# Kernel optimization log

Hardware: AMD Instinct MI355X
Metric: run time of the kernel (lower is better)

Reference implementation:

```python
import jax, jax.numpy as jnp
import numpy as np

B, T, X, H, Z, G, Y = 4096, 32, 256, 256, 256, 128, 2


def _xavier(key, fan_in, fan_out):
    lim = float(np.sqrt(6.0 / (fan_in + fan_out)))
    return jax.random.uniform(key, (fan_in, fan_out), jnp.float32, -lim, lim)


def setup_inputs() -> dict:
    key = jax.random.key(0)
    ks = jax.random.split(key, 18)
    return {
        "x": jax.random.normal(ks[0], (B, T, X), jnp.float32),
        "y_ph": jax.random.uniform(ks[1], (B, T, Y), jnp.float32),
        "T_ph": jax.random.randint(ks[2], (B,), 1, T + 1),  # 1..T valid days
        "h0": jnp.tanh(jax.random.normal(ks[3], (B, H), jnp.float32)),   # tanh(randn) init state
        "z0": jnp.tanh(jax.random.normal(ks[4], (B, Z), jnp.float32)),
        "eps": jax.random.normal(ks[5], (T, B, Z), jnp.float32),          # reparam noise per step
        # gate / candidate nets: fan_in = x + h + z
        "Wr": _xavier(ks[6], X + H + Z, H), "br": jnp.zeros((H,), jnp.float32),
        "Wu": _xavier(ks[7], X + H + Z, H), "bu": jnp.zeros((H,), jnp.float32),
        "Wh": _xavier(ks[8], X + H + Z, H), "bh": jnp.zeros((H,), jnp.float32),
        # prior latent net: fan_in = x + h
        "Wzp": _xavier(ks[9], X + H, Z), "bzp": jnp.zeros((Z,), jnp.float32),
        "Wpm": _xavier(ks[10], Z, Z), "bpm": jnp.zeros((Z,), jnp.float32),
        "Wps": _xavier(ks[11], Z, Z), "bps": jnp.zeros((Z,), jnp.float32),
        # posterior latent net: fan_in = x + h + y
        "Wzq": _xavier(ks[12], X + H + Y, Z), "bzq": jnp.zeros((Z,), jnp.float32),
        "Wqm": _xavier(ks[13], Z, Z), "bqm": jnp.zeros((Z,), jnp.float32),
        "Wqs": _xavier(ks[14], Z, Z), "bqs": jnp.zeros((Z,), jnp.float32),
        # output nets
        "Wg": _xavier(ks[15], X + H + Z, G), "bg": jnp.zeros((G,), jnp.float32),
        "Wy": _xavier(ks[16], G, Y), "by": jnp.zeros((Y,), jnp.float32),
    }


def reference(x, y_ph, T_ph, h0, z0, eps,
              Wr, br, Wu, bu, Wh, bh,
              Wzp, bzp, Wpm, bpm, Wps, bps,
              Wzq, bzq, Wqm, bqm, Wqs, bqs,
              Wg, bg, Wy, by):
    x_t = jnp.transpose(x, (1, 0, 2))     # [T, B, X]
    y_t = jnp.transpose(y_ph, (1, 0, 2))  # [T, B, Y]

    def step(carry, inp):
        h_prev, z_prev = carry
        xt, yt, et = inp
        ga = jnp.concatenate([xt, h_prev, z_prev], axis=-1)
        r = jax.nn.sigmoid(ga @ Wr + br)
        u = jax.nn.sigmoid(ga @ Wu + bu)
        ha = jnp.concatenate([xt, r * h_prev, z_prev], axis=-1)
        h_tilde = jnp.tanh(ha @ Wh + bh)
        h = (1.0 - u) * h_prev + u * h_tilde
        # prior p(z_t | x_t, h_t): z_prior = mean (is_prior=True)
        hzp = jnp.tanh(jnp.concatenate([xt, h], axis=-1) @ Wzp + bzp)
        mu_p = hzp @ Wpm + bpm
        sd_p = jnp.sqrt(jnp.exp(hzp @ Wps + bps))
        z_prior = mu_p
        # posterior q(z_t | x_t, h_t, y_t): reparameterized sample
        hzq = jnp.tanh(jnp.concatenate([xt, h, yt], axis=-1) @ Wzq + bzq)
        mu_q = hzq @ Wqm + bqm
        sd_q = jnp.sqrt(jnp.exp(hzq @ Wqs + bqs))
        z_post = mu_q + sd_q * et
        # KL(q || p) for diagonal Normals
        kl = jnp.log(sd_p / sd_q) + (sd_q ** 2 + (mu_q - mu_p) ** 2) / (2.0 * sd_p ** 2) - 0.5
        return (h, z_post), (h, z_post, z_prior, kl)

    (_, _), (h_s, z_post, z_prior, kl) = jax.lax.scan(step, (h0, z0), (x_t, y_t, eps))
    h_s = jnp.transpose(h_s, (1, 0, 2))      # [B, T, H]
    z_post = jnp.transpose(z_post, (1, 0, 2))
    kl = jnp.transpose(kl, (1, 0, 2)).sum(axis=-1)  # [B, T]

    g = jnp.tanh(jnp.concatenate([x, h_s, z_post], axis=-1) @ Wg + bg)  # [B, T, G]
    y = jax.nn.softmax(g @ Wy + by, axis=-1)                             # [B, T, Y]
    g_T = g[jnp.arange(x.shape[0]), T_ph - 1]                            # [B, G] (training, daily_att)
    return (y, kl, g_T)
```

## Files before the change

kernel.cpp:

```cpp
#include <hip/hip_runtime.h>

typedef unsigned short u16;
typedef unsigned int u32;
typedef __attribute__((ext_vector_type(8))) short short8;
typedef __attribute__((ext_vector_type(4))) float float4v;
typedef __attribute__((ext_vector_type(2))) float float2v;

#define B_SZ 4096
#define T_SZ 32
#define XD 256
#define HD 256
#define ZD 256
#define GD 128
#define YD 2

#define BM 64
#define NW 16

#define W1_OFF 0
#define W2_OFF 393216
#define W3_OFF 589824
#define W4_OFF 868352
#define WG_OFF 1130496
#define WTOT   1228800

#define YTOT  (B_SZ*T_SZ*YD)
#define KLTOT (B_SZ*T_SZ)

#define UST 264

__device__ __forceinline__ u16 f2bf(float f) {
    u32 u = __float_as_uint(f);
    u32 r = (u + 0x7fffu + ((u >> 16) & 1u)) >> 16;
    return (u16)r;
}
__device__ __forceinline__ float bf2f(u16 h) {
    return __uint_as_float(((u32)h) << 16);
}
__device__ __forceinline__ float tanh_f(float x) {
    float e = __expf(2.f * x);
    return 1.f - 2.f / (e + 1.f);
}
__device__ __forceinline__ float sigm_f(float x) {
    return 1.f / (1.f + __expf(-x));
}

__device__ __forceinline__ int aga_off(int r, int k) {
    return (((r >> 4) * 24 + (k >> 5)) << 9) + ((((k >> 3) & 3) * 16 + (r & 15)) << 3) + (k & 7);
}
__device__ __forceinline__ int a3h_off(int r, int k, int pq) {
    return (((pq * 2 + (r >> 4)) * 8 + (k >> 5)) << 9) + ((((k >> 3) & 3) * 16 + (r & 15)) << 3) + (k & 7);
}

#define MFMA(a, b, c) __builtin_amdgcn_mfma_f32_16x16x32_bf16(a, b, c, 0, 0, 0)

__global__ void prep_weights(const float* __restrict__ Wr, const float* __restrict__ Wu,
                             const float* __restrict__ Wh, const float* __restrict__ Wzp,
                             const float* __restrict__ Wzq, const float* __restrict__ Wpm,
                             const float* __restrict__ Wps, const float* __restrict__ Wqm,
                             const float* __restrict__ Wqs, const float* __restrict__ Wg,
                             u16* __restrict__ wts)
{
    int o = blockIdx.x * 256 + threadIdx.x;
    if (o >= WTOT) return;
    int mat, w, KT;
    if (o < W2_OFF)      { mat = 0; w = o;          KT = 24; }
    else if (o < W3_OFF) { mat = 1; w = o - W2_OFF; KT = 24; }
    else if (o < W4_OFF) { mat = 2; w = o - W3_OFF; KT = 17; }
    else if (o < WG_OFF) { mat = 3; w = o - W4_OFF; KT = 8;  }
    else                 { mat = 4; w = o - WG_OFF; KT = 24; }
    int nt  = w / (KT * 512);
    int rem = w - nt * (KT * 512);
    int kt  = rem >> 9;
    int q   = rem & 511;
    int lane = q >> 3, j = q & 7;
    int n = (nt << 4) | (lane & 15);
    int k = (kt << 5) + ((lane >> 4) << 3) + j;
    float v = 0.f;
    switch (mat) {
        case 0: v = (n < 256) ? Wr[k * 256 + n] : Wu[k * 256 + (n - 256)]; break;
        case 1: v = Wh[k * 256 + n]; break;
        case 2: v = (n < 256) ? (k < 512 ? Wzp[k * 256 + n] : 0.f)
                              : (k < 514 ? Wzq[k * 256 + (n - 256)] : 0.f); break;
        case 3: { int sel = n >> 8; int nn = n & 255;
                  const float* s = (sel == 0) ? Wpm : (sel == 1) ? Wps : (sel == 2) ? Wqm : Wqs;
                  v = s[k * 256 + nn]; } break;
        default: v = Wg[k * 128 + n]; break;
    }
    wts[o] = f2bf(v);
}

__global__ __launch_bounds__(1024, 4) void vrnn_all(
    const float* __restrict__ x,   const float* __restrict__ y_ph,
    const int*   __restrict__ Tph, const float* __restrict__ h0,
    const float* __restrict__ z0,  const float* __restrict__ eps,
    const float* __restrict__ br,  const float* __restrict__ bu,
    const float* __restrict__ bh,  const float* __restrict__ bzp,
    const float* __restrict__ bpm, const float* __restrict__ bps,
    const float* __restrict__ bzq, const float* __restrict__ bqm,
    const float* __restrict__ bqs, const float* __restrict__ bg,
    const float* __restrict__ by,  const float* __restrict__ Wy,
    const u16*   __restrict__ wts, float* __restrict__ out)
{
    __shared__ __align__(16) u16   a_ga[96 * 512];
    __shared__ __align__(16) u16   a3u[16896];
    __shared__ float part[8 * BM * 2];
    __shared__ float kl_acc[BM];
    __shared__ int   tph_s[BM];

    const int tid  = threadIdx.x;
    const int wv   = tid >> 6;
    const int lane = tid & 63;
    const int quad = lane >> 4;
    const int l15  = lane & 15;
    const int b0   = blockIdx.x * BM;

    const int c10 = wv * 32 + l15;
    const float bs1_0 = (c10 < 256) ? br[c10] : bu[c10 - 256];
    const float bs1_1 = (c10 + 16 < 256) ? br[c10 + 16] : bu[c10 + 16 - 256];
    const int c2  = wv * 16 + l15;
    const float bh_r  = bh[c2];
    const float bzp_r = bzp[c2];
    const float bzq_r = bzq[c2];
    const float b4pm = bpm[c2], b4ps = bps[c2], b4qm = bqm[c2], b4qs = bqs[c2];
    const int c5  = (wv >> 1) * 16 + l15;
    const int mt5 = wv & 1;
    const float bg_r = bg[c5];
    const float wy0 = Wy[c5 * 2], wy1 = Wy[c5 * 2 + 1];
    const float by0 = by[0], by1 = by[1];

    if (tid < BM) tph_s[tid] = Tph[b0 + tid];

    float h32r[16];
#pragma unroll
    for (int m = 0; m < 4; ++m)
#pragma unroll
        for (int i = 0; i < 4; ++i) {
            int row = m * 16 + quad * 4 + i;
            h32r[m * 4 + i] = __builtin_nontemporal_load(&h0[(size_t)(b0 + row) * HD + c2]);
        }

    const int sr  = tid >> 4;
    const int scc = (tid & 15) * 16;

    float4v xn[4];
    {
        const float* xp = &x[((size_t)(b0 + sr) * T_SZ + 0) * XD + scc];
#pragma unroll
        for (int q = 0; q < 4; ++q) xn[q] = __builtin_nontemporal_load((const float4v*)(xp + q * 4));

        const float* hp = &h0[(size_t)(b0 + sr) * HD + scc];
        const float* zp = &z0[(size_t)(b0 + sr) * ZD + scc];
        float4v hv[4], zv[4];
#pragma unroll
        for (int q = 0; q < 4; ++q) {
            hv[q] = __builtin_nontemporal_load((const float4v*)(hp + q * 4));
            zv[q] = __builtin_nontemporal_load((const float4v*)(zp + q * 4));
        }
        short8 hs0, hs1, zs0, zs1;
#pragma unroll
        for (int j = 0; j < 4; ++j) {
            hs0[j] = (short)f2bf(hv[0][j]); hs0[4 + j] = (short)f2bf(hv[1][j]);
            hs1[j] = (short)f2bf(hv[2][j]); hs1[4 + j] = (short)f2bf(hv[3][j]);
            zs0[j] = (short)f2bf(zv[0][j]); zs0[4 + j] = (short)f2bf(zv[1][j]);
            zs1[j] = (short)f2bf(zv[2][j]); zs1[4 + j] = (short)f2bf(zv[3][j]);
        }
        *(short8*)&a_ga[aga_off(sr, 256 + scc)]     = hs0;
        *(short8*)&a_ga[aga_off(sr, 256 + scc + 8)] = hs1;
        *(short8*)&a_ga[aga_off(sr, 512 + scc)]     = zs0;
        *(short8*)&a_ga[aga_off(sr, 512 + scc + 8)] = zs1;
    }
    __syncthreads();

    const float4v zero4 = {0.f, 0.f, 0.f, 0.f};
    float yA0 = 0.f, yA1 = 0.f, yB0 = 0.f, yB1 = 0.f, klA = 0.f, klB = 0.f;

    for (int t = 0; t < T_SZ; ++t) {
        {
            short8 s0, s1;
#pragma unroll
            for (int j = 0; j < 4; ++j) {
                s0[j] = (short)f2bf(xn[0][j]); s0[4 + j] = (short)f2bf(xn[1][j]);
                s1[j] = (short)f2bf(xn[2][j]); s1[4 + j] = (short)f2bf(xn[3][j]);
            }
            *(short8*)&a_ga[aga_off(sr, scc)]     = s0;
            *(short8*)&a_ga[aga_off(sr, scc + 8)] = s1;
        }
        __syncthreads();

        {
            const u16* pB0 = wts + W1_OFF + (((2 * wv    ) * 24) << 9) + lane * 8;
            const u16* pB1 = wts + W1_OFF + (((2 * wv + 1) * 24) << 9) + lane * 8;
            short8 r0[2], r1[2];
            r0[0] = *(const short8*)pB0;         r1[0] = *(const short8*)pB1;
            r0[1] = *(const short8*)(pB0 + 512); r1[1] = *(const short8*)(pB1 + 512);
            float4v a0[4], a1[4];
#pragma unroll
            for (int m = 0; m < 4; ++m) { a0[m] = zero4; a1[m] = zero4; }
#pragma unroll
            for (int kt = 0; kt < 24; ++kt) {
                short8 bc0 = r0[kt & 1], bc1 = r1[kt & 1];
                if (kt + 2 < 24) {
                    r0[kt & 1] = *(const short8*)(pB0 + ((kt + 2) << 9));
                    r1[kt & 1] = *(const short8*)(pB1 + ((kt + 2) << 9));
                }
#pragma unroll
                for (int m = 0; m < 4; ++m) {
                    short8 aF = *(const short8*)&a_ga[((m * 24 + kt) << 9) + lane * 8];
                    a0[m] = MFMA(aF, bc0, a0[m]);
                    a1[m] = MFMA(aF, bc1, a1[m]);
                }
            }
            __syncthreads();
#pragma unroll
            for (int m = 0; m < 4; ++m)
#pragma unroll
                for (int i = 0; i < 4; ++i) {
                    int row = m * 16 + quad * 4 + i;
                    {
                        float v = a0[m][i];
                        if (c10 < 256) {
                            int o = aga_off(row, 256 + c10);
                            float rr = sigm_f(v + bs1_0);
                            a_ga[o] = f2bf(rr * bf2f(a_ga[o]));
                        } else {
                            a3u[row * UST + (c10 - 256)] = f2bf(sigm_f(v + bs1_0));
                        }
                    }
                    {
                        int c = c10 + 16;
                        float v = a1[m][i];
                        if (c < 256) {
                            int o = aga_off(row, 256 + c);
                            float rr = sigm_f(v + bs1_1);
                            a_ga[o] = f2bf(rr * bf2f(a_ga[o]));
                        } else {
                            a3u[row * UST + (c - 256)] = f2bf(sigm_f(v + bs1_1));
                        }
                    }
                }
            __syncthreads();
        }

        {
            const u16* pB = wts + W2_OFF + ((wv * 24) << 9) + lane * 8;
            short8 rr2[2];
            rr2[0] = *(const short8*)pB; rr2[1] = *(const short8*)(pB + 512);
            float4v a[4];
#pragma unroll
            for (int m = 0; m < 4; ++m) a[m] = zero4;
#pragma unroll
            for (int kt = 0; kt < 24; ++kt) {
                short8 bc = rr2[kt & 1];
                if (kt + 2 < 24) rr2[kt & 1] = *(const short8*)(pB + ((kt + 2) << 9));
#pragma unroll
                for (int m = 0; m < 4; ++m) {
                    short8 aF = *(const short8*)&a_ga[((m * 24 + kt) << 9) + lane * 8];
                    a[m] = MFMA(aF, bc, a[m]);
                }
            }
            __syncthreads();
#pragma unroll
            for (int m = 0; m < 4; ++m)
#pragma unroll
                for (int i = 0; i < 4; ++i) {
                    int row = m * 16 + quad * 4 + i;
                    float ht = tanh_f(a[m][i] + bh_r);
                    float uu = bf2f(a3u[row * UST + c2]);
                    float h  = (1.f - uu) * h32r[m * 4 + i] + uu * ht;
                    h32r[m * 4 + i] = h;
                    a_ga[aga_off(row, 256 + c2)] = f2bf(h);
                }
            if (tid < 256) {
                int r = tid >> 2, grp = tid & 3;
                short8 v = {0, 0, 0, 0, 0, 0, 0, 0};
                if (grp == 0) {
                    const float* yp = &y_ph[((size_t)(b0 + r) * T_SZ + t) * YD];
                    v[0] = (short)f2bf(__builtin_nontemporal_load(yp));
                    v[1] = (short)f2bf(__builtin_nontemporal_load(yp + 1));
                }
                *(short8*)&a_ga[aga_off(r, 512 + grp * 8)] = v;
            }
            __syncthreads();
        }

#pragma unroll
        for (int half = 0; half < 2; ++half) {
            {
                const u16* pBp = wts + W3_OFF + ((wv * 17) << 9) + lane * 8;
                const u16* pBq = wts + W3_OFF + (((16 + wv) * 17) << 9) + lane * 8;
                short8 rp[2], rq[2];
                rp[0] = *(const short8*)pBp; rp[1] = *(const short8*)(pBp + 512);
                rq[0] = *(const short8*)pBq; rq[1] = *(const short8*)(pBq + 512);
                float4v aP[2], aQ[2];
                aP[0] = zero4; aP[1] = zero4; aQ[0] = zero4; aQ[1] = zero4;
#pragma unroll
                for (int kt = 0; kt < 17; ++kt) {
                    short8 bq = rq[kt & 1];
                    short8 bp = rp[kt & 1];
                    if (kt + 2 < 17) rq[kt & 1] = *(const short8*)(pBq + ((kt + 2) << 9));
                    if (kt + 2 < 16) rp[kt & 1] = *(const short8*)(pBp + ((kt + 2) << 9));
#pragma unroll
                    for (int m2 = 0; m2 < 2; ++m2) {
                        short8 aF = *(const short8*)&a_ga[(((half * 2 + m2) * 24 + kt) << 9) + lane * 8];
                        aQ[m2] = MFMA(aF, bq, aQ[m2]);
                        if (kt < 16) aP[m2] = MFMA(aF, bp, aP[m2]);
                    }
                }
                if (half == 0 && tid < BM) kl_acc[tid] = 0.f;
#pragma unroll
                for (int m2 = 0; m2 < 2; ++m2)
#pragma unroll
                    for (int i = 0; i < 4; ++i) {
                        int r5 = m2 * 16 + quad * 4 + i;
                        a3u[a3h_off(r5, c2, 0)] = f2bf(tanh_f(aP[m2][i] + bzp_r));
                        a3u[a3h_off(r5, c2, 1)] = f2bf(tanh_f(aQ[m2][i] + bzq_r));
                    }
                __syncthreads();
            }
            {
                const u16* pB0 = wts + W4_OFF + (((      wv) * 8) << 9) + lane * 8;
                const u16* pB1 = wts + W4_OFF + (((16 + wv) * 8) << 9) + lane * 8;
                const u16* pB2 = wts + W4_OFF + (((32 + wv) * 8) << 9) + lane * 8;
                const u16* pB3 = wts + W4_OFF + (((48 + wv) * 8) << 9) + lane * 8;
                float er8[8];
#pragma unroll
                for (int m2 = 0; m2 < 2; ++m2)
#pragma unroll
                    for (int i = 0; i < 4; ++i) {
                        int row = half * 32 + m2 * 16 + quad * 4 + i;
                        er8[m2 * 4 + i] = __builtin_nontemporal_load(
                            &eps[((size_t)t * B_SZ + (b0 + row)) * ZD + c2]);
                    }
                short8 r0[2], r1[2], r2[2], r3[2];
                r0[0] = *(const short8*)pB0;         r1[0] = *(const short8*)pB1;
                r2[0] = *(const short8*)pB2;         r3[0] = *(const short8*)pB3;
                r0[1] = *(const short8*)(pB0 + 512); r1[1] = *(const short8*)(pB1 + 512);
                r2[1] = *(const short8*)(pB2 + 512); r3[1] = *(const short8*)(pB3 + 512);
                float4v amp[2], asp[2], amq[2], asq[2];
                amp[0] = zero4; amp[1] = zero4; asp[0] = zero4; asp[1] = zero4;
                amq[0] = zero4; amq[1] = zero4; asq[0] = zero4; asq[1] = zero4;
#pragma unroll
                for (int kt = 0; kt < 8; ++kt) {
                    short8 b0c = r0[kt & 1], b1c = r1[kt & 1];
                    short8 b2c = r2[kt & 1], b3c = r3[kt & 1];
                    if (kt + 2 < 8) {
                        r0[kt & 1] = *(const short8*)(pB0 + ((kt + 2) << 9));
                        r1[kt & 1] = *(const short8*)(pB1 + ((kt + 2) << 9));
                        r2[kt & 1] = *(const short8*)(pB2 + ((kt + 2) << 9));
                        r3[kt & 1] = *(const short8*)(pB3 + ((kt + 2) << 9));
                    }
#pragma unroll
                    for (int m2 = 0; m2 < 2; ++m2) {
                        short8 aP = *(const short8*)&a3u[(((m2    ) * 8 + kt) << 9) + lane * 8];
                        short8 aQ = *(const short8*)&a3u[(((2 + m2) * 8 + kt) << 9) + lane * 8];
                        amp[m2] = MFMA(aP, b0c, amp[m2]); asp[m2] = MFMA(aP, b1c, asp[m2]);
                        amq[m2] = MFMA(aQ, b2c, amq[m2]); asq[m2] = MFMA(aQ, b3c, asq[m2]);
                    }
                }
#pragma unroll
                for (int m2 = 0; m2 < 2; ++m2)
#pragma unroll
                    for (int i = 0; i < 4; ++i) {
                        int row = half * 32 + m2 * 16 + quad * 4 + i;
                        float mp = amp[m2][i] + b4pm;
                        float sp = asp[m2][i] + b4ps;
                        float mq = amq[m2][i] + b4qm;
                        float sq = asq[m2][i] + b4qs;
                        float zpost = mq + __expf(0.5f * sq) * er8[m2 * 4 + i];
                        float dmu = mq - mp;
                        float kl = 0.5f * (sp - sq)
                                 + (__expf(sq) + dmu * dmu) * 0.5f * __expf(-sp) - 0.5f;
                        a_ga[aga_off(row, 512 + c2)] = f2bf(zpost);
                        kl += __shfl_xor(kl, 1); kl += __shfl_xor(kl, 2);
                        kl += __shfl_xor(kl, 4); kl += __shfl_xor(kl, 8);
                        if (l15 == 0) atomicAdd(&kl_acc[row], kl);
                    }
                __syncthreads();
            }
        }
        if ((tid & 15) == (t >> 1)) {
            float k = kl_acc[tid >> 4];
            if ((t & 1) == 0) klA = k; else klB = k;
        }

        {
            if (t + 1 < T_SZ) {
                const float* xp = &x[((size_t)(b0 + sr) * T_SZ + (t + 1)) * XD + scc];
#pragma unroll
                for (int q = 0; q < 4; ++q)
                    xn[q] = __builtin_nontemporal_load((const float4v*)(xp + q * 4));
            }
            const u16* pB = wts + WG_OFF + (((wv >> 1) * 24) << 9) + lane * 8;
            short8 rg[2];
            rg[0] = *(const short8*)pB; rg[1] = *(const short8*)(pB + 512);
            float4v a5[2];
            a5[0] = zero4; a5[1] = zero4;
#pragma unroll
            for (int kt = 0; kt < 24; ++kt) {
                short8 bc = rg[kt & 1];
                if (kt + 2 < 24) rg[kt & 1] = *(const short8*)(pB + ((kt + 2) << 9));
                short8 aFa = *(const short8*)&a_ga[(((mt5    ) * 24 + kt) << 9) + lane * 8];
                short8 aFb = *(const short8*)&a_ga[(((mt5 + 2) * 24 + kt) << 9) + lane * 8];
                a5[0] = MFMA(aFa, bc, a5[0]);
                a5[1] = MFMA(aFb, bc, a5[1]);
            }
#pragma unroll
            for (int half = 0; half < 2; ++half) {
                int m = mt5 + 2 * half;
#pragma unroll
                for (int i = 0; i < 4; ++i) {
                    int row = m * 16 + quad * 4 + i;
                    float g = tanh_f(a5[half][i] + bg_r);
                    if (tph_s[row] - 1 == t)
                        __builtin_nontemporal_store(g,
                            &out[YTOT + KLTOT + (size_t)(b0 + row) * GD + c5]);
                    float p0 = g * wy0, p1 = g * wy1;
                    p0 += __shfl_xor(p0, 1); p0 += __shfl_xor(p0, 2);
                    p0 += __shfl_xor(p0, 4); p0 += __shfl_xor(p0, 8);
                    p1 += __shfl_xor(p1, 1); p1 += __shfl_xor(p1, 2);
                    p1 += __shfl_xor(p1, 4); p1 += __shfl_xor(p1, 8);
                    if (l15 == 0) {
                        part[((wv >> 1) * BM + row) * 2]     = p0;
                        part[((wv >> 1) * BM + row) * 2 + 1] = p1;
                    }
                }
            }
            __syncthreads();
            if ((tid & 15) == (t >> 1)) {
                int r = tid >> 4;
                float s0 = by0, s1 = by1;
#pragma unroll
                for (int j = 0; j < 8; ++j) {
                    s0 += part[(j * BM + r) * 2];
                    s1 += part[(j * BM + r) * 2 + 1];
                }
                float mx = fmaxf(s0, s1);
                float e0 = __expf(s0 - mx), e1 = __expf(s1 - mx);
                float inv = 1.f / (e0 + e1);
                if ((t & 1) == 0) { yA0 = e0 * inv; yA1 = e1 * inv; }
                else              { yB0 = e0 * inv; yB1 = e1 * inv; }
            }
        }
    }

    {
        int r = tid >> 4, tt = tid & 15;
        float4v yv = {yA0, yA1, yB0, yB1};
        __builtin_nontemporal_store(yv,
            (float4v*)&out[((size_t)(b0 + r) * T_SZ + tt * 2) * YD]);
        float2v kv = {klA, klB};
        __builtin_nontemporal_store(kv,
            (float2v*)&out[YTOT + (size_t)(b0 + r) * T_SZ + tt * 2]);
    }
}

extern "C" void kernel_launch(void* const* d_in, const int* in_sizes, int n_in,
                              void* d_out, int out_size, void* d_ws, size_t ws_size,
                              hipStream_t stream)
{
    const float* x   = (const float*)d_in[0];
    const float* yph = (const float*)d_in[1];
    const int*   Tph = (const int*)  d_in[2];
    const float* h0  = (const float*)d_in[3];
    const float* z0  = (const float*)d_in[4];
    const float* eps = (const float*)d_in[5];
    const float* Wr  = (const float*)d_in[6];
    const float* br  = (const float*)d_in[7];
    const float* Wu  = (const float*)d_in[8];
    const float* bu  = (const float*)d_in[9];
    const float* Wh  = (const float*)d_in[10];
    const float* bh  = (const float*)d_in[11];
    const float* Wzp = (const float*)d_in[12];
    const float* bzp = (const float*)d_in[13];
    const float* Wpm = (const float*)d_in[14];
    const float* bpm = (const float*)d_in[15];
    const float* Wps = (const float*)d_in[16];
    const float* bps = (const float*)d_in[17];
    const float* Wzq = (const float*)d_in[18];
    const float* bzq = (const float*)d_in[19];
    const float* Wqm = (const float*)d_in[20];
    const float* bqm = (const float*)d_in[21];
    const float* Wqs = (const float*)d_in[22];
    const float* bqs = (const float*)d_in[23];
    const float* Wg  = (const float*)d_in[24];
    const float* bg  = (const float*)d_in[25];
    const float* Wy  = (const float*)d_in[26];
    const float* by  = (const float*)d_in[27];
    u16*   wts = (u16*)d_ws;
    float* out = (float*)d_out;

    hipLaunchKernelGGL(prep_weights, dim3((WTOT + 255) / 256), dim3(256), 0, stream,
                       Wr, Wu, Wh, Wzp, Wzq, Wpm, Wps, Wqm, Wqs, Wg, wts);
    hipLaunchKernelGGL(vrnn_all, dim3(B_SZ / BM), dim3(1024), 0, stream,
                       x, yph, Tph, h0, z0, eps, br, bu, bh, bzp, bpm, bps,
                       bzq, bqm, bqs, bg, by, Wy, wts, out);
}
```

Baseline: 4.662 ms.

## Halve batch tile to 32 rows with 8 waves, widening per-wave column tiles

Each block now handles 32 batch rows with 512 threads (8 waves) instead of 64 rows with 1024 threads. Each wave covers twice as many output columns, and the weight-prefetch depth grows from 2 to 4 k-steps. The posterior/prior stage now runs in one pass instead of two halves. This doubles the grid and is meant to improve occupancy and latency hiding of the sequential per-step GEMMs. The cost is that weight traffic per batch row doubles, since each block re-streams the full weight set for half as many rows, and register pressure rises.

```diff
diff --git a/kernel.cpp b/kernel.cpp
--- a/kernel.cpp
+++ b/kernel.cpp
@@ -14,8 +14,8 @@
 #define GD 128
 #define YD 2
 
-#define BM 64
-#define NW 16
+#define BM 32
+#define NW 8
 
 #define W1_OFF 0
 #define W2_OFF 393216
@@ -48,7 +48,7 @@
 __device__ __forceinline__ int aga_off(int r, int k) {
     return (((r >> 4) * 24 + (k >> 5)) << 9) + ((((k >> 3) & 3) * 16 + (r & 15)) << 3) + (k & 7);
 }
-__device__ __forceinline__ int a3h_off(int r, int k, int pq) {
+__device__ __forceinline__ int a3s_off(int r, int k, int pq) {
     return (((pq * 2 + (r >> 4)) * 8 + (k >> 5)) << 9) + ((((k >> 3) & 3) * 16 + (r & 15)) << 3) + (k & 7);
 }
 
@@ -90,7 +90,7 @@
     wts[o] = f2bf(v);
 }
 
-__global__ __launch_bounds__(1024, 4) void vrnn_all(
+__global__ __launch_bounds__(512, 2) void vrnn_all(
     const float* __restrict__ x,   const float* __restrict__ y_ph,
     const int*   __restrict__ Tph, const float* __restrict__ h0,
     const float* __restrict__ z0,  const float* __restrict__ eps,
@@ -102,9 +102,9 @@
     const float* __restrict__ by,  const float* __restrict__ Wy,
     const u16*   __restrict__ wts, float* __restrict__ out)
 {
-    __shared__ __align__(16) u16   a_ga[96 * 512];
-    __shared__ __align__(16) u16   a3u[16896];
-    __shared__ float part[8 * BM * 2];
+    __shared__ __align__(16) u16   a_ga[48 * 512];
+    __shared__ __align__(16) u16   a3s[32 * 512];
+    __shared__ float part[NW * BM * 2];
     __shared__ float kl_acc[BM];
     __shared__ int   tph_s[BM];
 
@@ -115,30 +115,40 @@
     const int l15  = lane & 15;
     const int b0   = blockIdx.x * BM;
 
-    const int c10 = wv * 32 + l15;
-    const float bs1_0 = (c10 < 256) ? br[c10] : bu[c10 - 256];
-    const float bs1_1 = (c10 + 16 < 256) ? br[c10 + 16] : bu[c10 + 16 - 256];
-    const int c2  = wv * 16 + l15;
-    const float bh_r  = bh[c2];
-    const float bzp_r = bzp[c2];
-    const float bzq_r = bzq[c2];
-    const float b4pm = bpm[c2], b4ps = bps[c2], b4qm = bqm[c2], b4qs = bqs[c2];
-    const int c5  = (wv >> 1) * 16 + l15;
-    const int mt5 = wv & 1;
+    const int c1b = 64 * wv + l15;
+    float bs1[4];
+#pragma unroll
+    for (int nt = 0; nt < 4; ++nt) {
+        int c = c1b + nt * 16;
+        bs1[nt] = (c < 256) ? br[c] : bu[c - 256];
+    }
+    const int c2a = 32 * wv + l15;
+    const int c2b = c2a + 16;
+    const float bh_a  = bh[c2a],  bh_b  = bh[c2b];
+    const float bzp_a = bzp[c2a], bzp_b = bzp[c2b];
+    const float bzq_a = bzq[c2a], bzq_b = bzq[c2b];
+    const float bpm_a = bpm[c2a], bpm_b = bpm[c2b];
+    const float bps_a = bps[c2a], bps_b = bps[c2b];
+    const float bqm_a = bqm[c2a], bqm_b = bqm[c2b];
+    const float bqs_a = bqs[c2a], bqs_b = bqs[c2b];
+    const int c5  = 16 * wv + l15;
     const float bg_r = bg[c5];
     const float wy0 = Wy[c5 * 2], wy1 = Wy[c5 * 2 + 1];
     const float by0 = by[0], by1 = by[1];
 
     if (tid < BM) tph_s[tid] = Tph[b0 + tid];
 
-    float h32r[16];
-#pragma unroll
-    for (int m = 0; m < 4; ++m)
-#pragma unroll
-        for (int i = 0; i < 4; ++i) {
-            int row = m * 16 + quad * 4 + i;
-            h32r[m * 4 + i] = __builtin_nontemporal_load(&h0[(size_t)(b0 + row) * HD + c2]);
-        }
+    float h32r[2][2][4];
+#pragma unroll
+    for (int ct = 0; ct < 2; ++ct)
+#pragma unroll
+        for (int mt = 0; mt < 2; ++mt)
+#pragma unroll
+            for (int i = 0; i < 4; ++i) {
+                int row = mt * 16 + quad * 4 + i;
+                int c = ct ? c2b : c2a;
+                h32r[ct][mt][i] = __builtin_nontemporal_load(&h0[(size_t)(b0 + row) * HD + c]);
+            }
 
     const int sr  = tid >> 4;
     const int scc = (tid & 15) * 16;
@@ -189,89 +199,98 @@
         __syncthreads();
 
         {
-            const u16* pB0 = wts + W1_OFF + (((2 * wv    ) * 24) << 9) + lane * 8;
-            const u16* pB1 = wts + W1_OFF + (((2 * wv + 1) * 24) << 9) + lane * 8;
-            short8 r0[2], r1[2];
-            r0[0] = *(const short8*)pB0;         r1[0] = *(const short8*)pB1;
-            r0[1] = *(const short8*)(pB0 + 512); r1[1] = *(const short8*)(pB1 + 512);
-            float4v a0[4], a1[4];
-#pragma unroll
-            for (int m = 0; m < 4; ++m) { a0[m] = zero4; a1[m] = zero4; }
+            const u16* pB[4];
+#pragma unroll
+            for (int nt = 0; nt < 4; ++nt)
+                pB[nt] = wts + W1_OFF + (((4 * wv + nt) * 24) << 9) + lane * 8;
+            short8 rg[4][4];
+#pragma unroll
+            for (int d = 0; d < 4; ++d)
+#pragma unroll
+                for (int nt = 0; nt < 4; ++nt)
+                    rg[nt][d] = *(const short8*)(pB[nt] + (d << 9));
+            float4v ac[4][2];
+#pragma unroll
+            for (int nt = 0; nt < 4; ++nt) { ac[nt][0] = zero4; ac[nt][1] = zero4; }
 #pragma unroll
             for (int kt = 0; kt < 24; ++kt) {
-                short8 bc0 = r0[kt & 1], bc1 = r1[kt & 1];
-                if (kt + 2 < 24) {
-                    r0[kt & 1] = *(const short8*)(pB0 + ((kt + 2) << 9));
-                    r1[kt & 1] = *(const short8*)(pB1 + ((kt + 2) << 9));
-                }
-#pragma unroll
-                for (int m = 0; m < 4; ++m) {
-                    short8 aF = *(const short8*)&a_ga[((m * 24 + kt) << 9) + lane * 8];
-                    a0[m] = MFMA(aF, bc0, a0[m]);
-                    a1[m] = MFMA(aF, bc1, a1[m]);
-                }
-            }
-            __syncthreads();
-#pragma unroll
-            for (int m = 0; m < 4; ++m)
-#pragma unroll
-                for (int i = 0; i < 4; ++i) {
-                    int row = m * 16 + quad * 4 + i;
-                    {
-                        float v = a0[m][i];
-                        if (c10 < 256) {
-                            int o = aga_off(row, 256 + c10);
-                            float rr = sigm_f(v + bs1_0);
-                            a_ga[o] = f2bf(rr * bf2f(a_ga[o]));
-                        } else {
-                            a3u[row * UST + (c10 - 256)] = f2bf(sigm_f(v + bs1_0));
-                        }
-                    }
-                    {
-                        int c = c10 + 16;
-                        float v = a1[m][i];
+                short8 aF0 = *(const short8*)&a_ga[(kt << 9) + lane * 8];
+                short8 aF1 = *(const short8*)&a_ga[((24 + kt) << 9) + lane * 8];
+                short8 b0c = rg[0][kt & 3], b1c = rg[1][kt & 3];
+                short8 b2c = rg[2][kt & 3], b3c = rg[3][kt & 3];
+                if (kt + 4 < 24) {
+#pragma unroll
+                    for (int nt = 0; nt < 4; ++nt)
+                        rg[nt][kt & 3] = *(const short8*)(pB[nt] + ((kt + 4) << 9));
+                }
+                ac[0][0] = MFMA(aF0, b0c, ac[0][0]); ac[0][1] = MFMA(aF1, b0c, ac[0][1]);
+                ac[1][0] = MFMA(aF0, b1c, ac[1][0]); ac[1][1] = MFMA(aF1, b1c, ac[1][1]);
+                ac[2][0] = MFMA(aF0, b2c, ac[2][0]); ac[2][1] = MFMA(aF1, b2c, ac[2][1]);
+                ac[3][0] = MFMA(aF0, b3c, ac[3][0]); ac[3][1] = MFMA(aF1, b3c, ac[3][1]);
+            }
+            __syncthreads();
+#pragma unroll
+            for (int nt = 0; nt < 4; ++nt) {
+                int c = c1b + nt * 16;
+#pragma unroll
+                for (int mt = 0; mt < 2; ++mt)
+#pragma unroll
+                    for (int i = 0; i < 4; ++i) {
+                        int row = mt * 16 + quad * 4 + i;
+                        float s = sigm_f(ac[nt][mt][i] + bs1[nt]);
                         if (c < 256) {
                             int o = aga_off(row, 256 + c);
-                            float rr = sigm_f(v + bs1_1);
-                            a_ga[o] = f2bf(rr * bf2f(a_ga[o]));
+                            a_ga[o] = f2bf(s * bf2f(a_ga[o]));
                         } else {
-                            a3u[row * UST + (c - 256)] = f2bf(sigm_f(v + bs1_1));
+                            a3s[row * UST + (c - 256)] = f2bf(s);
                         }
                     }
-                }
+            }
             __syncthreads();
         }
 
         {
-            const u16* pB = wts + W2_OFF + ((wv * 24) << 9) + lane * 8;
-            short8 rr2[2];
-            rr2[0] = *(const short8*)pB; rr2[1] = *(const short8*)(pB + 512);
-            float4v a[4];
-#pragma unroll
-            for (int m = 0; m < 4; ++m) a[m] = zero4;
+            const u16* pB[2];
+            pB[0] = wts + W2_OFF + (((2 * wv    ) * 24) << 9) + lane * 8;
+            pB[1] = wts + W2_OFF + (((2 * wv + 1) * 24) << 9) + lane * 8;
+            short8 rg[2][4];
+#pragma unroll
+            for (int d = 0; d < 4; ++d) {
+                rg[0][d] = *(const short8*)(pB[0] + (d << 9));
+                rg[1][d] = *(const short8*)(pB[1] + (d << 9));
+            }
+            float4v ac[2][2];
+            ac[0][0] = zero4; ac[0][1] = zero4; ac[1][0] = zero4; ac[1][1] = zero4;
 #pragma unroll
             for (int kt = 0; kt < 24; ++kt) {
-                short8 bc = rr2[kt & 1];
-                if (kt + 2 < 24) rr2[kt & 1] = *(const short8*)(pB + ((kt + 2) << 9));
-#pragma unroll
-                for (int m = 0; m < 4; ++m) {
-                    short8 aF = *(const short8*)&a_ga[((m * 24 + kt) << 9) + lane * 8];
-                    a[m] = MFMA(aF, bc, a[m]);
-                }
-            }
-            __syncthreads();
-#pragma unroll
-            for (int m = 0; m < 4; ++m)
-#pragma unroll
-                for (int i = 0; i < 4; ++i) {
-                    int row = m * 16 + quad * 4 + i;
-                    float ht = tanh_f(a[m][i] + bh_r);
-                    float uu = bf2f(a3u[row * UST + c2]);
-                    float h  = (1.f - uu) * h32r[m * 4 + i] + uu * ht;
-                    h32r[m * 4 + i] = h;
-                    a_ga[aga_off(row, 256 + c2)] = f2bf(h);
-                }
-            if (tid < 256) {
+                short8 aF0 = *(const short8*)&a_ga[(kt << 9) + lane * 8];
+                short8 aF1 = *(const short8*)&a_ga[((24 + kt) << 9) + lane * 8];
+                short8 b0c = rg[0][kt & 3], b1c = rg[1][kt & 3];
+                if (kt + 4 < 24) {
+                    rg[0][kt & 3] = *(const short8*)(pB[0] + ((kt + 4) << 9));
+                    rg[1][kt & 3] = *(const short8*)(pB[1] + ((kt + 4) << 9));
+                }
+                ac[0][0] = MFMA(aF0, b0c, ac[0][0]); ac[0][1] = MFMA(aF1, b0c, ac[0][1]);
+                ac[1][0] = MFMA(aF0, b1c, ac[1][0]); ac[1][1] = MFMA(aF1, b1c, ac[1][1]);
+            }
+            __syncthreads();
+#pragma unroll
+            for (int ct = 0; ct < 2; ++ct) {
+                int c = ct ? c2b : c2a;
+                float bhv = ct ? bh_b : bh_a;
+#pragma unroll
+                for (int mt = 0; mt < 2; ++mt)
+#pragma unroll
+                    for (int i = 0; i < 4; ++i) {
+                        int row = mt * 16 + quad * 4 + i;
+                        float ht = tanh_f(ac[ct][mt][i] + bhv);
+                        float uu = bf2f(a3s[row * UST + c]);
+                        float h  = (1.f - uu) * h32r[ct][mt][i] + uu * ht;
+                        h32r[ct][mt][i] = h;
+                        a_ga[aga_off(row, 256 + c)] = f2bf(h);
+                    }
+            }
+            if (tid < 128) {
                 int r = tid >> 2, grp = tid & 3;
                 short8 v = {0, 0, 0, 0, 0, 0, 0, 0};
                 if (grp == 0) {
@@ -284,104 +303,151 @@
             __syncthreads();
         }
 
-#pragma unroll
-        for (int half = 0; half < 2; ++half) {
-            {
-                const u16* pBp = wts + W3_OFF + ((wv * 17) << 9) + lane * 8;
-                const u16* pBq = wts + W3_OFF + (((16 + wv) * 17) << 9) + lane * 8;
-                short8 rp[2], rq[2];
-                rp[0] = *(const short8*)pBp; rp[1] = *(const short8*)(pBp + 512);
-                rq[0] = *(const short8*)pBq; rq[1] = *(const short8*)(pBq + 512);
-                float4v aP[2], aQ[2];
-                aP[0] = zero4; aP[1] = zero4; aQ[0] = zero4; aQ[1] = zero4;
-#pragma unroll
-                for (int kt = 0; kt < 17; ++kt) {
-                    short8 bq = rq[kt & 1];
-                    short8 bp = rp[kt & 1];
-                    if (kt + 2 < 17) rq[kt & 1] = *(const short8*)(pBq + ((kt + 2) << 9));
-                    if (kt + 2 < 16) rp[kt & 1] = *(const short8*)(pBp + ((kt + 2) << 9));
-#pragma unroll
-                    for (int m2 = 0; m2 < 2; ++m2) {
-                        short8 aF = *(const short8*)&a_ga[(((half * 2 + m2) * 24 + kt) << 9) + lane * 8];
-                        aQ[m2] = MFMA(aF, bq, aQ[m2]);
-                        if (kt < 16) aP[m2] = MFMA(aF, bp, aP[m2]);
-                    }
-                }
-                if (half == 0 && tid < BM) kl_acc[tid] = 0.f;
-#pragma unroll
-                for (int m2 = 0; m2 < 2; ++m2)
+        {
+            const u16* pP[2]; const u16* pQ[2];
+            pP[0] = wts + W3_OFF + (((2 * wv    ) * 17) << 9) + lane * 8;
+            pP[1] = wts + W3_OFF + (((2 * wv + 1) * 17) << 9) + lane * 8;
+            pQ[0] = wts + W3_OFF + (((16 + 2 * wv    ) * 17) << 9) + lane * 8;
+            pQ[1] = wts + W3_OFF + (((16 + 2 * wv + 1) * 17) << 9) + lane * 8;
+            short8 rp[2][4], rq[2][4];
+#pragma unroll
+            for (int d = 0; d < 4; ++d) {
+                rp[0][d] = *(const short8*)(pP[0] + (d << 9));
+                rp[1][d] = *(const short8*)(pP[1] + (d << 9));
+                rq[0][d] = *(const short8*)(pQ[0] + (d << 9));
+                rq[1][d] = *(const short8*)(pQ[1] + (d << 9));
+            }
+            float4v aP[2][2], aQ[2][2];
+            aP[0][0] = zero4; aP[0][1] = zero4; aP[1][0] = zero4; aP[1][1] = zero4;
+            aQ[0][0] = zero4; aQ[0][1] = zero4; aQ[1][0] = zero4; aQ[1][1] = zero4;
+#pragma unroll
+            for (int kt = 0; kt < 17; ++kt) {
+                short8 aF0 = *(const short8*)&a_ga[(kt << 9) + lane * 8];
+                short8 aF1 = *(const short8*)&a_ga[((24 + kt) << 9) + lane * 8];
+                short8 bq0 = rq[0][kt & 3], bq1 = rq[1][kt & 3];
+                if (kt + 4 < 17) {
+                    rq[0][kt & 3] = *(const short8*)(pQ[0] + ((kt + 4) << 9));
+                    rq[1][kt & 3] = *(const short8*)(pQ[1] + ((kt + 4) << 9));
+                }
+                aQ[0][0] = MFMA(aF0, bq0, aQ[0][0]); aQ[0][1] = MFMA(aF1, bq0, aQ[0][1]);
+                aQ[1][0] = MFMA(aF0, bq1, aQ[1][0]); aQ[1][1] = MFMA(aF1, bq1, aQ[1][1]);
+                if (kt < 16) {
+                    short8 bp0 = rp[0][kt & 3], bp1 = rp[1][kt & 3];
+                    if (kt + 4 < 16) {
+                        rp[0][kt & 3] = *(const short8*)(pP[0] + ((kt + 4) << 9));
+                        rp[1][kt & 3] = *(const short8*)(pP[1] + ((kt + 4) << 9));
+                    }
+                    aP[0][0] = MFMA(aF0, bp0, aP[0][0]); aP[0][1] = MFMA(aF1, bp0, aP[0][1]);
+                    aP[1][0] = MFMA(aF0, bp1, aP[1][0]); aP[1][1] = MFMA(aF1, bp1, aP[1][1]);
+                }
+            }
+            if (tid < BM) kl_acc[tid] = 0.f;
+#pragma unroll
+            for (int ct = 0; ct < 2; ++ct) {
+                int c = ct ? c2b : c2a;
+                float bzpv = ct ? bzp_b : bzp_a;
+                float bzqv = ct ? bzq_b : bzq_a;
+#pragma unroll
+                for (int mt = 0; mt < 2; ++mt)
 #pragma unroll
                     for (int i = 0; i < 4; ++i) {
-                        int r5 = m2 * 16 + quad * 4 + i;
-                        a3u[a3h_off(r5, c2, 0)] = f2bf(tanh_f(aP[m2][i] + bzp_r));
-                        a3u[a3h_off(r5, c2, 1)] = f2bf(tanh_f(aQ[m2][i] + bzq_r));
-                    }
-                __syncthreads();
-            }
-            {
-                const u16* pB0 = wts + W4_OFF + (((      wv) * 8) << 9) + lane * 8;
-                const u16* pB1 = wts + W4_OFF + (((16 + wv) * 8) << 9) + lane * 8;
-                const u16* pB2 = wts + W4_OFF + (((32 + wv) * 8) << 9) + lane * 8;
-                const u16* pB3 = wts + W4_OFF + (((48 + wv) * 8) << 9) + lane * 8;
-                float er8[8];
-#pragma unroll
-                for (int m2 = 0; m2 < 2; ++m2)
+                        int row = mt * 16 + quad * 4 + i;
+                        a3s[a3s_off(row, c, 0)] = f2bf(tanh_f(aP[ct][mt][i] + bzpv));
+                        a3s[a3s_off(row, c, 1)] = f2bf(tanh_f(aQ[ct][mt][i] + bzqv));
+                    }
+            }
+            __syncthreads();
+        }
+
+        {
+            float er[2][2][4];
+#pragma unroll
+            for (int ct = 0; ct < 2; ++ct)
+#pragma unroll
+                for (int mt = 0; mt < 2; ++mt)
 #pragma unroll
                     for (int i = 0; i < 4; ++i) {
-                        int row = half * 32 + m2 * 16 + quad * 4 + i;
-                        er8[m2 * 4 + i] = __builtin_nontemporal_load(
-                            &eps[((size_t)t * B_SZ + (b0 + row)) * ZD + c2]);
-                    }
-                short8 r0[2], r1[2], r2[2], r3[2];
-                r0[0] = *(const short8*)pB0;         r1[0] = *(const short8*)pB1;
-                r2[0] = *(const short8*)pB2;         r3[0] = *(const short8*)pB3;
-                r0[1] = *(const short8*)(pB0 + 512); r1[1] = *(const short8*)(pB1 + 512);
-                r2[1] = *(const short8*)(pB2 + 512); r3[1] = *(const short8*)(pB3 + 512);
-                float4v amp[2], asp[2], amq[2], asq[2];
-                amp[0] = zero4; amp[1] = zero4; asp[0] = zero4; asp[1] = zero4;
-                amq[0] = zero4; amq[1] = zero4; asq[0] = zero4; asq[1] = zero4;
-#pragma unroll
-                for (int kt = 0; kt < 8; ++kt) {
-                    short8 b0c = r0[kt & 1], b1c = r1[kt & 1];
-                    short8 b2c = r2[kt & 1], b3c = r3[kt & 1];
-                    if (kt + 2 < 8) {
-                        r0[kt & 1] = *(const short8*)(pB0 + ((kt + 2) << 9));
-                        r1[kt & 1] = *(const short8*)(pB1 + ((kt + 2) << 9));
-                        r2[kt & 1] = *(const short8*)(pB2 + ((kt + 2) << 9));
-                        r3[kt & 1] = *(const short8*)(pB3 + ((kt + 2) << 9));
-                    }
-#pragma unroll
-                    for (int m2 = 0; m2 < 2; ++m2) {
-                        short8 aP = *(const short8*)&a3u[(((m2    ) * 8 + kt) << 9) + lane * 8];
-                        short8 aQ = *(const short8*)&a3u[(((2 + m2) * 8 + kt) << 9) + lane * 8];
-                        amp[m2] = MFMA(aP, b0c, amp[m2]); asp[m2] = MFMA(aP, b1c, asp[m2]);
-                        amq[m2] = MFMA(aQ, b2c, amq[m2]); asq[m2] = MFMA(aQ, b3c, asq[m2]);
-                    }
-                }
-#pragma unroll
-                for (int m2 = 0; m2 < 2; ++m2)
+                        int row = mt * 16 + quad * 4 + i;
+                        int c = ct ? c2b : c2a;
+                        er[ct][mt][i] = __builtin_nontemporal_load(
+                            &eps[((size_t)t * B_SZ + (b0 + row)) * ZD + c]);
+                    }
+            const u16* p4[8];
+#pragma unroll
+            for (int h = 0; h < 4; ++h)
+#pragma unroll
+                for (int ct = 0; ct < 2; ++ct)
+                    p4[h * 2 + ct] = wts + W4_OFF + (((h * 16 + 2 * wv + ct) * 8) << 9) + lane * 8;
+            short8 r4[8][2];
+#pragma unroll
+            for (int s = 0; s < 8; ++s) {
+                r4[s][0] = *(const short8*)p4[s];
+                r4[s][1] = *(const short8*)(p4[s] + 512);
+            }
+            float4v ac[8][2];
+#pragma unroll
+            for (int s = 0; s < 8; ++s) { ac[s][0] = zero4; ac[s][1] = zero4; }
+#pragma unroll
+            for (int kt = 0; kt < 8; ++kt) {
+                short8 aP0 = *(const short8*)&a3s[((     kt) << 9) + lane * 8];
+                short8 aP1 = *(const short8*)&a3s[(( 8 + kt) << 9) + lane * 8];
+                short8 aQ0 = *(const short8*)&a3s[((16 + kt) << 9) + lane * 8];
+                short8 aQ1 = *(const short8*)&a3s[((24 + kt) << 9) + lane * 8];
+                short8 bc[8];
+#pragma unroll
+                for (int s = 0; s < 8; ++s) {
+                    bc[s] = r4[s][kt & 1];
+                    if (kt + 2 < 8) r4[s][kt & 1] = *(const short8*)(p4[s] + ((kt + 2) << 9));
+                }
+                ac[0][0] = MFMA(aP0, bc[0], ac[0][0]); ac[0][1] = MFMA(aP1, bc[0], ac[0][1]);
+                ac[1][0] = MFMA(aP0, bc[1], ac[1][0]); ac[1][1] = MFMA(aP1, bc[1], ac[1][1]);
+                ac[2][0] = MFMA(aP0, bc[2], ac[2][0]); ac[2][1] = MFMA(aP1, bc[2], ac[2][1]);
+                ac[3][0] = MFMA(aP0, bc[3], ac[3][0]); ac[3][1] = MFMA(aP1, bc[3], ac[3][1]);
+                ac[4][0] = MFMA(aQ0, bc[4], ac[4][0]); ac[4][1] = MFMA(aQ1, bc[4], ac[4][1]);
+                ac[5][0] = MFMA(aQ0, bc[5], ac[5][0]); ac[5][1] = MFMA(aQ1, bc[5], ac[5][1]);
+                ac[6][0] = MFMA(aQ0, bc[6], ac[6][0]); ac[6][1] = MFMA(aQ1, bc[6], ac[6][1]);
+                ac[7][0] = MFMA(aQ0, bc[7], ac[7][0]); ac[7][1] = MFMA(aQ1, bc[7], ac[7][1]);
+            }
+            float kl2[2][4];
+#pragma unroll
+            for (int mt = 0; mt < 2; ++mt)
+#pragma unroll
+                for (int i = 0; i < 4; ++i) kl2[mt][i] = 0.f;
+#pragma unroll
+            for (int ct = 0; ct < 2; ++ct) {
+                int c = ct ? c2b : c2a;
+                float vpm = ct ? bpm_b : bpm_a, vps = ct ? bps_b : bps_a;
+                float vqm = ct ? bqm_b : bqm_a, vqs = ct ? bqs_b : bqs_a;
+#pragma unroll
+                for (int mt = 0; mt < 2; ++mt)
 #pragma unroll
                     for (int i = 0; i < 4; ++i) {
-                        int row = half * 32 + m2 * 16 + quad * 4 + i;
-                        float mp = amp[m2][i] + b4pm;
-                        float sp = asp[m2][i] + b4ps;
-                        float mq = amq[m2][i] + b4qm;
-                        float sq = asq[m2][i] + b4qs;
-                        float zpost = mq + __expf(0.5f * sq) * er8[m2 * 4 + i];
+                        int row = mt * 16 + quad * 4 + i;
+                        float mp = ac[0 + ct][mt][i] + vpm;
+                        float sp = ac[2 + ct][mt][i] + vps;
+                        float mq = ac[4 + ct][mt][i] + vqm;
+                        float sq = ac[6 + ct][mt][i] + vqs;
+                        float zpost = mq + __expf(0.5f * sq) * er[ct][mt][i];
                         float dmu = mq - mp;
-                        float kl = 0.5f * (sp - sq)
-                                 + (__expf(sq) + dmu * dmu) * 0.5f * __expf(-sp) - 0.5f;
-                        a_ga[aga_off(row, 512 + c2)] = f2bf(zpost);
-                        kl += __shfl_xor(kl, 1); kl += __shfl_xor(kl, 2);
-                        kl += __shfl_xor(kl, 4); kl += __shfl_xor(kl, 8);
-                        if (l15 == 0) atomicAdd(&kl_acc[row], kl);
-                    }
-                __syncthreads();
-            }
-        }
-        if ((tid & 15) == (t >> 1)) {
-            float k = kl_acc[tid >> 4];
-            if ((t & 1) == 0) klA = k; else klB = k;
+                        kl2[mt][i] += 0.5f * (sp - sq)
+                                    + (__expf(sq) + dmu * dmu) * 0.5f * __expf(-sp) - 0.5f;
+                        a_ga[aga_off(row, 512 + c)] = f2bf(zpost);
+                    }
+            }
+#pragma unroll
+            for (int mt = 0; mt < 2; ++mt)
+#pragma unroll
+                for (int i = 0; i < 4; ++i) {
+                    float v = kl2[mt][i];
+                    v += __shfl_xor(v, 1); v += __shfl_xor(v, 2);
+                    v += __shfl_xor(v, 4); v += __shfl_xor(v, 8);
+                    if (l15 == 0) atomicAdd(&kl_acc[mt * 16 + quad * 4 + i], v);
+                }
+            __syncthreads();
+            if ((tid & 15) == (t >> 1)) {
+                float k = kl_acc[tid >> 4];
+                if ((t & 1) == 0) klA = k; else klB = k;
+            }
         }
 
         {
@@ -391,27 +457,28 @@
                 for (int q = 0; q < 4; ++q)
                     xn[q] = __builtin_nontemporal_load((const float4v*)(xp + q * 4));
             }
-            const u16* pB = wts + WG_OFF + (((wv >> 1) * 24) << 9) + lane * 8;
-            short8 rg[2];
-            rg[0] = *(const short8*)pB; rg[1] = *(const short8*)(pB + 512);
+            const u16* pB = wts + WG_OFF + ((wv * 24) << 9) + lane * 8;
+            short8 rg[4];
+#pragma unroll
+            for (int d = 0; d < 4; ++d)
+                rg[d] = *(const short8*)(pB + (d << 9));
             float4v a5[2];
             a5[0] = zero4; a5[1] = zero4;
 #pragma unroll
             for (int kt = 0; kt < 24; ++kt) {
-                short8 bc = rg[kt & 1];
-                if (kt + 2 < 24) rg[kt & 1] = *(const short8*)(pB + ((kt + 2) << 9));
-                short8 aFa = *(const short8*)&a_ga[(((mt5    ) * 24 + kt) << 9) + lane * 8];
-                short8 aFb = *(const short8*)&a_ga[(((mt5 + 2) * 24 + kt) << 9) + lane * 8];
-                a5[0] = MFMA(aFa, bc, a5[0]);
-                a5[1] = MFMA(aFb, bc, a5[1]);
-            }
-#pragma unroll
-            for (int half = 0; half < 2; ++half) {
-                int m = mt5 + 2 * half;
+                short8 bc = rg[kt & 3];
+                if (kt + 4 < 24) rg[kt & 3] = *(const short8*)(pB + ((kt + 4) << 9));
+                short8 aF0 = *(const short8*)&a_ga[(kt << 9) + lane * 8];
+                short8 aF1 = *(const short8*)&a_ga[((24 + kt) << 9) + lane * 8];
+                a5[0] = MFMA(aF0, bc, a5[0]);
+                a5[1] = MFMA(aF1, bc, a5[1]);
+            }
+#pragma unroll
+            for (int mt = 0; mt < 2; ++mt)
 #pragma unroll
                 for (int i = 0; i < 4; ++i) {
-                    int row = m * 16 + quad * 4 + i;
-                    float g = tanh_f(a5[half][i] + bg_r);
+                    int row = mt * 16 + quad * 4 + i;
+                    float g = tanh_f(a5[mt][i] + bg_r);
                     if (tph_s[row] - 1 == t)
                         __builtin_nontemporal_store(g,
                             &out[YTOT + KLTOT + (size_t)(b0 + row) * GD + c5]);
@@ -421,17 +488,16 @@
                     p1 += __shfl_xor(p1, 1); p1 += __shfl_xor(p1, 2);
                     p1 += __shfl_xor(p1, 4); p1 += __shfl_xor(p1, 8);
                     if (l15 == 0) {
-                        part[((wv >> 1) * BM + row) * 2]     = p0;
-                        part[((wv >> 1) * BM + row) * 2 + 1] = p1;
-                    }
-                }
-            }
+                        part[(wv * BM + row) * 2]     = p0;
+                        part[(wv * BM + row) * 2 + 1] = p1;
+                    }
+                }
             __syncthreads();
             if ((tid & 15) == (t >> 1)) {
                 int r = tid >> 4;
                 float s0 = by0, s1 = by1;
 #pragma unroll
-                for (int j = 0; j < 8; ++j) {
+                for (int j = 0; j < NW; ++j) {
                     s0 += part[(j * BM + r) * 2];
                     s1 += part[(j * BM + r) * 2 + 1];
                 }
@@ -492,7 +558,7 @@
 
     hipLaunchKernelGGL(prep_weights, dim3((WTOT + 255) / 256), dim3(256), 0, stream,
                        Wr, Wu, Wh, Wzp, Wzq, Wpm, Wps, Wqm, Wqs, Wg, wts);
-    hipLaunchKernelGGL(vrnn_all, dim3(B_SZ / BM), dim3(1024), 0, stream,
+    hipLaunchKernelGGL(vrnn_all, dim3(B_SZ / BM), dim3(512), 0, stream,
                        x, yph, Tph, h0, z0, eps, br, bu, bh, bzp, bpm, bps,
                        bzq, bqm, bqs, bg, by, Wy, wts, out);
 }
```

New measurement: 4.687 ms. Within noise of the previous version (+0.5%).
